# Optimization experiments

Measured on AMD Instinct MI355X. Metric: run time of the kernel, lower is better.

## Reference

```python
import jax, jax.numpy as jnp
import numpy as np

N, E, H, HEADS, L = 10000, 64000, 128, 8, 8
D = H // HEADS
CUTOFF = 5.0
EPS = 1e-5


def _xavier(key, shape):
    lim = float(np.sqrt(6.0 / (shape[0] + shape[1])))
    return jax.random.uniform(key, shape, minval=-lim, maxval=lim, dtype=jnp.float32)


def setup_inputs() -> dict:
    key = jax.random.key(0)
    ks = jax.random.split(key, 20)
    zeros = lambda *s: jnp.zeros(s, jnp.float32)
    return {
        "x": jax.random.normal(ks[0], (N, H), jnp.float32),
        "vec": 0.1 * jax.random.normal(ks[1], (N, L, H), jnp.float32),
        "f_ij": jax.random.normal(ks[2], (E, H), jnp.float32),
        "d_ij": jax.random.normal(ks[3], (E, L), jnp.float32),
        "r_ij": jax.random.uniform(ks[4], (E,), jnp.float32, 0.0, CUTOFF),
        "edge_index": jax.random.randint(ks[5], (2, E), 0, N),
        "ln_g": jnp.ones((H,), jnp.float32), "ln_b": zeros(H),
        "vln_w": jnp.ones((H,), jnp.float32),
        "W_vec": _xavier(ks[6], (H, 3 * H)),
        "W_q": _xavier(ks[7], (H, H)), "b_q": zeros(H),
        "W_k": _xavier(ks[8], (H, H)), "b_k": zeros(H),
        "W_v": _xavier(ks[9], (H, H)), "b_v": zeros(H),
        "W_dk": _xavier(ks[10], (H, H)), "b_dk": zeros(H),
        "W_dv": _xavier(ks[11], (H, H)), "b_dv": zeros(H),
        "W_s": _xavier(ks[12], (H, 2 * H)), "b_s": zeros(2 * H),
        "W_f": _xavier(ks[13], (H, H)), "b_f": zeros(H),
        "W_src": _xavier(ks[14], (H, H)),
        "W_trg": _xavier(ks[15], (H, H)),
        "W_o": _xavier(ks[16], (H, 3 * H)), "b_o": zeros(3 * H),
    }


def _layernorm(x, g, b):
    mu = jnp.mean(x, -1, keepdims=True)
    var = jnp.mean((x - mu) ** 2, -1, keepdims=True)
    return (x - mu) * jax.lax.rsqrt(var + EPS) * g + b


def _cutoff(r):
    # CosineCutoff: 0.5*(cos(pi*r/cutoff)+1) for r < cutoff
    return 0.5 * (jnp.cos(jnp.pi * r / CUTOFF) + 1.0) * (r < CUTOFF).astype(r.dtype)


def _vec_rejection(v, d):
    # v: [E, L, H], d: [E, L]; remove the component of v along d (per channel)
    proj = jnp.einsum("elh,el->eh", v, d)
    return v - proj[:, None, :] * d[:, :, None]


def reference(x, vec, f_ij, d_ij, r_ij, edge_index, ln_g, ln_b, vln_w, W_vec,
              W_q, b_q, W_k, b_k, W_v, b_v, W_dk, b_dk, W_dv, b_dv,
              W_s, b_s, W_f, b_f, W_src, W_trg, W_o, b_o):
    src, dst = edge_index[0], edge_index[1]  # j (source), i (target)
    x = _layernorm(x, ln_g, ln_b)
    vec = vec * vln_w  # VecLayerNorm with norm_type="none": identity norm * weight

    q = (x @ W_q + b_q).reshape(N, HEADS, D)
    k = (x @ W_k + b_k).reshape(N, HEADS, D)
    v = (x @ W_v + b_v).reshape(N, HEADS, D)
    dk = jax.nn.silu(f_ij @ W_dk + b_dk).reshape(E, HEADS, D)
    dv = jax.nn.silu(f_ij @ W_dv + b_dv).reshape(E, HEADS, D)

    vec1, vec2, vec3 = jnp.split(jnp.einsum("nlh,hk->nlk", vec, W_vec), 3, axis=-1)
    vec_dot = jnp.sum(vec1 * vec2, axis=1)  # [N, H]

    # ---- message (per edge) ----
    attn = jnp.sum(q[dst] * k[src] * dk, axis=-1)          # [E, HEADS]
    attn = jax.nn.silu(attn) * _cutoff(r_ij)[:, None]
    vm = (v[src] * dv * attn[:, :, None]).reshape(E, H)    # [E, H]
    s1, s2 = jnp.split(jax.nn.silu(vm @ W_s + b_s), 2, axis=-1)
    vec_m = vec[src] * s1[:, None, :] + s2[:, None, :] * d_ij[:, :, None]  # [E, L, H]

    # ---- aggregate (scatter-add to target nodes) ----
    x_agg = jax.ops.segment_sum(vm, dst, num_segments=N)       # [N, H]
    vec_agg = jax.ops.segment_sum(vec_m, dst, num_segments=N)  # [N, L, H]

    # ---- edge update ----
    w1 = _vec_rejection(jnp.einsum("elh,hk->elk", vec[dst], W_trg), d_ij)
    w2 = _vec_rejection(jnp.einsum("elh,hk->elk", vec[src], W_src), -d_ij)
    w_dot = jnp.sum(w1 * w2, axis=1)                       # [E, H]
    df_ij = jax.nn.silu(f_ij @ W_f + b_f) * w_dot

    # ---- node update ----
    o1, o2, o3 = jnp.split(x_agg @ W_o + b_o, 3, axis=-1)
    dx = vec_dot * o2 + o3
    dvec = vec3 * o1[:, None, :] + vec_agg
    return dx, dvec, df_ij
```

## Files before the change

### kernel.cpp

```cpp
#include <hip/hip_runtime.h>
#include <hip/hip_bf16.h>
#include <math.h>

#define N_NODES 10000
#define N_EDGES 64000
#define H 128
#define L 8
#define NL (N_NODES * L)

typedef __attribute__((ext_vector_type(4))) float f32x4;
typedef __attribute__((ext_vector_type(8))) __bf16 bf16x8;
typedef __attribute__((ext_vector_type(4))) __bf16 bf16x4;

__device__ __forceinline__ float silu_f(float x) { return x / (1.f + __expf(-x)); }

__global__ __launch_bounds__(256) void prep_kernel(
    const float* __restrict__ Wvec, const float* __restrict__ Wq, const float* __restrict__ Wk,
    const float* __restrict__ Wv, const float* __restrict__ Wdk, const float* __restrict__ Wdv,
    const float* __restrict__ Ws, const float* __restrict__ Wtrg, const float* __restrict__ Wsrc,
    const float* __restrict__ Wf, const float* __restrict__ Wo,
    const float* __restrict__ bq, const float* __restrict__ bk, const float* __restrict__ bv,
    const float* __restrict__ bdk, const float* __restrict__ bdv, const float* __restrict__ bf,
    __bf16* __restrict__ Wt, float* __restrict__ bqkv, float* __restrict__ bfm,
    const float* __restrict__ x, const float* __restrict__ g, const float* __restrict__ b,
    __bf16* __restrict__ xln, const float* __restrict__ vec, const float* __restrict__ w,
    __bf16* __restrict__ vecw, __bf16* __restrict__ vecwT) {
  __shared__ float tile[32][33];
  int bid = blockIdx.x;
  int t = threadIdx.x;
  if (bid < 256) {
    int ct = bid >> 2, kt = bid & 3;
    int gc0 = ct * 32;
    const float* W; int ldw, sc0;
    if      (gc0 < 384)  { W = Wvec; ldw = 384; sc0 = gc0; }
    else if (gc0 < 512)  { W = Wtrg; ldw = 128; sc0 = gc0 - 384; }
    else if (gc0 < 640)  { W = Wsrc; ldw = 128; sc0 = gc0 - 512; }
    else if (gc0 < 768)  { W = Wq;   ldw = 128; sc0 = gc0 - 640; }
    else if (gc0 < 896)  { W = Wk;   ldw = 128; sc0 = gc0 - 768; }
    else if (gc0 < 1024) { W = Wv;   ldw = 128; sc0 = gc0 - 896; }
    else if (gc0 < 1152) { W = Wdk;  ldw = 128; sc0 = gc0 - 1024; }
    else if (gc0 < 1280) { W = Wdv;  ldw = 128; sc0 = gc0 - 1152; }
    else if (gc0 < 1408) { W = Wf;   ldw = 128; sc0 = gc0 - 1280; }
    else if (gc0 < 1664) { W = Ws;   ldw = 256; sc0 = gc0 - 1408; }
    else                 { W = Wo;   ldw = 384; sc0 = gc0 - 1664; }
    int tx = t & 31, ty = t >> 5;
#pragma unroll
    for (int i = 0; i < 4; ++i)
      tile[ty + i * 8][tx] = W[(size_t)(kt * 32 + ty + i * 8) * ldw + sc0 + tx];
    __syncthreads();
#pragma unroll
    for (int i = 0; i < 4; ++i)
      Wt[(size_t)(gc0 + ty + i * 8) * 128 + kt * 32 + tx] = (__bf16)tile[tx][ty + i * 8];
  } else if (bid == 256) {
    if (t < 128) { bqkv[t] = bq[t]; bqkv[128 + t] = bk[t]; bqkv[256 + t] = bv[t]; }
  } else if (bid == 257) {
    if (t < 128) { bfm[t] = bdk[t]; bfm[128 + t] = bdv[t]; bfm[256 + t] = bf[t]; }
  } else if (bid < 258 + 5000) {
    int n = (bid - 258) * 2 + (t >> 7);
    int h = t & 127;
    float wl = w[h];
    const float* base = vec + (size_t)n * 1024 + h;
    __bf16* orow = vecw + (size_t)n * 1024 + h;
    bf16x8 pack;
#pragma unroll
    for (int l = 0; l < 8; ++l) {
      __bf16 bv = (__bf16)(base[l * 128] * wl);
      orow[l * 128] = bv;
      pack[l] = bv;
    }
    *(bf16x8*)(vecwT + (size_t)n * 1024 + h * 8) = pack;
  } else {
    int wave = t >> 6;
    int lane = t & 63;
    int n = (bid - 258 - 5000) * 4 + wave;
    if (n >= N_NODES) return;
    const float* xr = x + (size_t)n * H;
    float a0 = xr[lane], a1 = xr[lane + 64];
    float s = a0 + a1;
#pragma unroll
    for (int off = 32; off >= 1; off >>= 1) s += __shfl_xor(s, off, 64);
    float mu = s * (1.f / H);
    float d0 = a0 - mu, d1 = a1 - mu;
    float v = d0 * d0 + d1 * d1;
#pragma unroll
    for (int off = 32; off >= 1; off >>= 1) v += __shfl_xor(v, off, 64);
    float rstd = rsqrtf(v * (1.f / H) + 1e-5f);
    __bf16* orow = xln + (size_t)n * H;
    orow[lane] = (__bf16)(d0 * rstd * g[lane] + b[lane]);
    orow[lane + 64] = (__bf16)(d1 * rstd * g[lane + 64] + b[lane + 64]);
  }
}

__global__ __launch_bounds__(256) void egather_kernel(const float* __restrict__ fin,
                                                      const float* __restrict__ d_ij,
                                                      const float* __restrict__ r_ij,
                                                      const int* __restrict__ elist,
                                                      __bf16* __restrict__ fout,
                                                      float* __restrict__ d2,
                                                      float* __restrict__ r2) {
  int bid = blockIdx.x;
  if (bid < 8000) {
    int p = bid * 8 + (threadIdx.x >> 5);
    int c = (threadIdx.x & 31) * 4;
    int e = elist[p];
    f32x4 a = *(const f32x4*)(fin + (size_t)e * 128 + c);
    bf16x4 h;
    h[0] = (__bf16)a[0]; h[1] = (__bf16)a[1]; h[2] = (__bf16)a[2]; h[3] = (__bf16)a[3];
    *(bf16x4*)(fout + (size_t)p * 128 + c) = h;
  } else {
    int idx = (bid - 8000) * 256 + threadIdx.x;
    int p = idx >> 3, j = idx & 7;
    int e = elist[p];
    d2[idx] = d_ij[(size_t)e * 8 + j];
    if (j == 0) r2[p] = r_ij[e];
  }
}

__global__ __launch_bounds__(256, 2) void vdot_gemm(const __bf16* __restrict__ A,
                                                    const __bf16* __restrict__ Bt,
                                                    float* __restrict__ vdot) {
  __shared__ __bf16 As[128 * 128];
  const int tid = threadIdx.x;
  const int lane = tid & 63;
  const int wave = tid >> 6;
  const int wm = wave >> 1, wn = wave & 1;
  const int row0 = blockIdx.x * 128;

#pragma unroll
  for (int i = 0; i < 8; ++i) {
    int c = tid + i * 256;
    int row = c >> 4, k8 = c & 15;
    int k8s = k8 ^ (row & 7);
    const __bf16* src = A + (size_t)(row0 + row) * 128 + k8s * 8;
    __builtin_amdgcn_global_load_lds((const __attribute__((address_space(1))) void*)src,
                                     (__attribute__((address_space(3))) void*)(As + c * 8),
                                     16, 0, 0);
  }
  __syncthreads();

  f32x4 pacc[4][4], acc[4][4];
#pragma unroll
  for (int mi = 0; mi < 4; ++mi)
#pragma unroll
    for (int ni = 0; ni < 4; ++ni) {
      pacc[mi][ni] = f32x4{0.f, 0.f, 0.f, 0.f};
      acc[mi][ni] = f32x4{0.f, 0.f, 0.f, 0.f};
    }
#pragma unroll
  for (int ct = 0; ct < 2; ++ct) {
    const __bf16* Bbase =
        Bt + ((size_t)(ct * 128 + wn * 64 + (lane & 15)) << 7) + ((lane >> 4) << 3);
#pragma unroll
    for (int ks = 0; ks < 4; ++ks) {
      bf16x8 b[4];
#pragma unroll
      for (int ni = 0; ni < 4; ++ni) b[ni] = *(const bf16x8*)(Bbase + (ni << 11) + (ks << 5));
      bf16x8 a[4];
#pragma unroll
      for (int mi = 0; mi < 4; ++mi) {
        int row = wm * 64 + mi * 16 + (lane & 15);
        int byte = (row * 256 + ks * 64 + ((lane >> 4) << 4)) ^ ((row & 7) << 4);
        a[mi] = *(const bf16x8*)((const char*)As + byte);
      }
      if (ct == 0) {
#pragma unroll
        for (int mi = 0; mi < 4; ++mi)
#pragma unroll
          for (int ni = 0; ni < 4; ++ni)
            pacc[mi][ni] =
                __builtin_amdgcn_mfma_f32_16x16x32_bf16(a[mi], b[ni], pacc[mi][ni], 0, 0, 0);
      } else {
#pragma unroll
        for (int mi = 0; mi < 4; ++mi)
#pragma unroll
          for (int ni = 0; ni < 4; ++ni)
            acc[mi][ni] =
                __builtin_amdgcn_mfma_f32_16x16x32_bf16(a[mi], b[ni], acc[mi][ni], 0, 0, 0);
      }
    }
  }
#pragma unroll
  for (int mi = 0; mi < 4; ++mi) {
#pragma unroll
    for (int ni = 0; ni < 4; ++ni) {
      float sr = pacc[mi][ni][0] * acc[mi][ni][0] + pacc[mi][ni][1] * acc[mi][ni][1] +
                 pacc[mi][ni][2] * acc[mi][ni][2] + pacc[mi][ni][3] * acc[mi][ni][3];
      sr += __shfl_xor(sr, 16, 64);
      if ((lane & 16) == 0) {
        int node = (row0 >> 3) + wm * 8 + mi * 2 + (lane >> 5);
        int col = wn * 64 + ni * 16 + (lane & 15);
        vdot[(size_t)node * 128 + col] = sr;
      }
    }
  }
}

__global__ __launch_bounds__(256, 3) void gemm_multi(
    const __bf16* __restrict__ vecw, const __bf16* __restrict__ xln,
    const __bf16* __restrict__ fijb, const __bf16* __restrict__ Wt,
    const float* __restrict__ bqkv, const float* __restrict__ bfm,
    __bf16* __restrict__ vec3, __bf16* __restrict__ vtT, __bf16* __restrict__ vsT,
    __bf16* __restrict__ qkv, __bf16* __restrict__ fm) {
  __shared__ __bf16 As[128 * 128];
  __bf16* Cs = As;
  const int tid = threadIdx.x;
  const int lane = tid & 63;
  const int wave = tid >> 6;
  const int wm = wave >> 1, wn = wave & 1;

  int bid = blockIdx.x;
  const __bf16* A;
  const __bf16* Bt;
  const float* bias = nullptr;
  __bf16* C = nullptr;
  int nx, ny, M, ldc = 384, act = 0, big = 0;
  if (bid < 1896) {
    A = vecw; Bt = Wt + (size_t)256 * 128; nx = 625; ny = 3; M = NL; big = 1;
  } else if (bid < 2136) {
    bid -= 1896;
    A = xln; Bt = Wt + (size_t)640 * 128; bias = bqkv; C = qkv; nx = 79; ny = 3; M = N_NODES;
  } else {
    bid -= 2136;
    A = fijb; Bt = Wt + (size_t)1024 * 128; bias = bfm; C = fm; nx = 500; ny = 3; M = N_EDGES;
    act = 1;
  }

  const int xi = bid & 7;
  const int rem = bid >> 3;
  const int y = rem % ny;
  const int x = (rem / ny) * 8 + xi;
  if (x >= nx) return;
  const int row0 = x * 128;

#pragma unroll
  for (int i = 0; i < 8; ++i) {
    int c = tid + i * 256;
    int row = c >> 4, k8 = c & 15;
    int k8s = k8 ^ (row & 7);
    const __bf16* src = A + (size_t)(row0 + row) * 128 + k8s * 8;
    __builtin_amdgcn_global_load_lds((const __attribute__((address_space(1))) void*)src,
                                     (__attribute__((address_space(3))) void*)(As + c * 8),
                                     16, 0, 0);
  }
  __syncthreads();

  const __bf16* Bbase =
      Bt + ((size_t)(y * 128 + wn * 64 + (lane & 15)) << 7) + ((lane >> 4) << 3);
  bf16x8 b[4][4];
#pragma unroll
  for (int ks = 0; ks < 4; ++ks)
#pragma unroll
    for (int ni = 0; ni < 4; ++ni) b[ks][ni] = *(const bf16x8*)(Bbase + (ni << 11) + (ks << 5));

  f32x4 acc[4][4];
#pragma unroll
  for (int mi = 0; mi < 4; ++mi)
#pragma unroll
    for (int ni = 0; ni < 4; ++ni) acc[mi][ni] = f32x4{0.f, 0.f, 0.f, 0.f};

#pragma unroll
  for (int ks = 0; ks < 4; ++ks) {
    bf16x8 a[4];
#pragma unroll
    for (int mi = 0; mi < 4; ++mi) {
      int row = wm * 64 + mi * 16 + (lane & 15);
      int byte = (row * 256 + ks * 64 + ((lane >> 4) << 4)) ^ ((row & 7) << 4);
      a[mi] = *(const bf16x8*)((const char*)As + byte);
    }
#pragma unroll
    for (int mi = 0; mi < 4; ++mi)
#pragma unroll
      for (int ni = 0; ni < 4; ++ni)
        acc[mi][ni] =
            __builtin_amdgcn_mfma_f32_16x16x32_bf16(a[mi], b[ks][ni], acc[mi][ni], 0, 0, 0);
  }

  if (big) {
    __bf16* T = (y == 1) ? vtT : vsT;
#pragma unroll
    for (int p = 0; p < 2; ++p) {
      __syncthreads();
      int rl = (wm << 5) | ((lane >> 4) << 2);
#pragma unroll
      for (int q = 0; q < 2; ++q) {
        int mi = 2 * p + q;
#pragma unroll
        for (int ni = 0; ni < 4; ++ni) {
          int col = wn * 64 + ni * 16 + (lane & 15);
#pragma unroll
          for (int r = 0; r < 4; ++r)
            Cs[(rl + q * 16 + r) * 136 + col] = (__bf16)acc[mi][ni][r];
        }
      }
      __syncthreads();
      if (y == 0) {
#pragma unroll
        for (int rr = 0; rr < 4; ++rr) {
          int row = (tid >> 4) + rr * 16;
          int chunk = tid & 15;
          bf16x8 v = *(const bf16x8*)(Cs + row * 136 + chunk * 8);
          int grow = row0 + (row >> 5) * 64 + (2 * p + ((row >> 4) & 1)) * 16 + (row & 15);
          *(bf16x8*)(vec3 + (size_t)grow * 128 + chunk * 8) = v;
        }
      } else {
#pragma unroll
        for (int j = 0; j < 4; ++j) {
          int idx = tid + 256 * j;
          int node_idx = idx >> 7;
          int h = idx & 127;
          int wmm = node_idx >> 2, qq = (node_idx >> 1) & 1, w = node_idx & 1;
          int base = wmm * 32 + qq * 16 + w * 8;
          bf16x8 v;
#pragma unroll
          for (int l = 0; l < 8; ++l) v[l] = Cs[(base + l) * 136 + h];
          int g = (row0 >> 3) + wmm * 8 + (2 * p + qq) * 2 + w;
          *(bf16x8*)(T + (size_t)g * 1024 + h * 8) = v;
        }
      }
    }
  } else {
    const int cstore = y * 128;
#pragma unroll
    for (int p = 0; p < 2; ++p) {
      __syncthreads();
      int rl = (wm << 5) | ((lane >> 4) << 2);
#pragma unroll
      for (int q = 0; q < 2; ++q) {
        int mi = 2 * p + q;
#pragma unroll
        for (int ni = 0; ni < 4; ++ni) {
          int col = wn * 64 + ni * 16 + (lane & 15);
          float bv = bias[cstore + col];
#pragma unroll
          for (int r = 0; r < 4; ++r) {
            float xv = acc[mi][ni][r] + bv;
            if (act) xv = silu_f(xv);
            Cs[(rl + q * 16 + r) * 136 + col] = (__bf16)xv;
          }
        }
      }
      __syncthreads();
#pragma unroll
      for (int rr = 0; rr < 4; ++rr) {
        int row = (tid >> 4) + rr * 16;
        int chunk = tid & 15;
        bf16x8 v = *(const bf16x8*)(Cs + row * 136 + chunk * 8);
        int grow = row0 + (row >> 5) * 64 + (2 * p + ((row >> 4) & 1)) * 16 + (row & 15);
        if (grow < M)
          *(bf16x8*)(C + (size_t)grow * ldc + cstore + chunk * 8) = v;
      }
    }
  }
}

template <typename CT>
__global__ __launch_bounds__(256, 3) void gemm_v9(const __bf16* __restrict__ A,
                                                  const __bf16* __restrict__ Bt,
                                                  const float* __restrict__ bias,
                                                  CT* __restrict__ C, int M, int nx, int ny,
                                                  int ldc, int act) {
  __shared__ __bf16 As[128 * 128];
  __bf16* Cs = As;
  const int bid = blockIdx.x;
  const int xi = bid & 7;
  const int rem = bid >> 3;
  const int y = rem % ny;
  const int x = (rem / ny) * 8 + xi;
  if (x >= nx) return;
  const int tid = threadIdx.x;
  const int lane = tid & 63;
  const int wave = tid >> 6;
  const int wm = wave >> 1, wn = wave & 1;
  const int row0 = x * 128;

#pragma unroll
  for (int i = 0; i < 8; ++i) {
    int c = tid + i * 256;
    int row = c >> 4, k8 = c & 15;
    int k8s = k8 ^ (row & 7);
    const __bf16* src = A + (size_t)(row0 + row) * 128 + k8s * 8;
    __builtin_amdgcn_global_load_lds((const __attribute__((address_space(1))) void*)src,
                                     (__attribute__((address_space(3))) void*)(As + c * 8),
                                     16, 0, 0);
  }
  __syncthreads();

  const __bf16* Bbase =
      Bt + ((size_t)(y * 128 + wn * 64 + (lane & 15)) << 7) + ((lane >> 4) << 3);
  bf16x8 b[4][4];
#pragma unroll
  for (int ks = 0; ks < 4; ++ks)
#pragma unroll
    for (int ni = 0; ni < 4; ++ni) b[ks][ni] = *(const bf16x8*)(Bbase + (ni << 11) + (ks << 5));

  f32x4 acc[4][4];
#pragma unroll
  for (int mi = 0; mi < 4; ++mi)
#pragma unroll
    for (int ni = 0; ni < 4; ++ni) acc[mi][ni] = f32x4{0.f, 0.f, 0.f, 0.f};

#pragma unroll
  for (int ks = 0; ks < 4; ++ks) {
    bf16x8 a[4];
#pragma unroll
    for (int mi = 0; mi < 4; ++mi) {
      int row = wm * 64 + mi * 16 + (lane & 15);
      int byte = (row * 256 + ks * 64 + ((lane >> 4) << 4)) ^ ((row & 7) << 4);
      a[mi] = *(const bf16x8*)((const char*)As + byte);
    }
#pragma unroll
    for (int mi = 0; mi < 4; ++mi)
#pragma unroll
      for (int ni = 0; ni < 4; ++ni)
        acc[mi][ni] =
            __builtin_amdgcn_mfma_f32_16x16x32_bf16(a[mi], b[ks][ni], acc[mi][ni], 0, 0, 0);
  }

  const int cstore = y * 128;
  if constexpr (sizeof(CT) == 2) {
#pragma unroll
    for (int p = 0; p < 2; ++p) {
      __syncthreads();
      int rl = (wm << 5) | ((lane >> 4) << 2);
#pragma unroll
      for (int q = 0; q < 2; ++q) {
        int mi = 2 * p + q;
#pragma unroll
        for (int ni = 0; ni < 4; ++ni) {
          int col = wn * 64 + ni * 16 + (lane & 15);
          float bv = bias ? bias[cstore + col] : 0.f;
#pragma unroll
          for (int r = 0; r < 4; ++r) {
            float xv = acc[mi][ni][r] + bv;
            if (act) xv = silu_f(xv);
            Cs[(rl + q * 16 + r) * 136 + col] = (__bf16)xv;
          }
        }
      }
      __syncthreads();
#pragma unroll
      for (int rr = 0; rr < 4; ++rr) {
        int row = (tid >> 4) + rr * 16;
        int chunk = tid & 15;
        bf16x8 v = *(const bf16x8*)(Cs + row * 136 + chunk * 8);
        int grow = row0 + (row >> 5) * 64 + (2 * p + ((row >> 4) & 1)) * 16 + (row & 15);
        if (grow < M)
          *(bf16x8*)(C + (size_t)grow * ldc + cstore + chunk * 8) = v;
      }
    }
  } else {
#pragma unroll
    for (int mi = 0; mi < 4; ++mi) {
      int rbase = row0 + wm * 64 + mi * 16 + ((lane >> 4) << 2);
#pragma unroll
      for (int ni = 0; ni < 4; ++ni) {
        int gcol = cstore + wn * 64 + ni * 16 + (lane & 15);
        float bv = bias ? bias[cstore + wn * 64 + ni * 16 + (lane & 15)] : 0.f;
#pragma unroll
        for (int r = 0; r < 4; ++r) {
          int grow = rbase + r;
          if (grow < M) {
            float xv = acc[mi][ni][r] + bv;
            if (act) xv = silu_f(xv);
            C[(size_t)grow * ldc + gcol] = (CT)xv;
          }
        }
      }
    }
  }
}

static inline int swz_grid(int nx, int ny) { return ((nx + 7) / 8) * ny * 8; }

__global__ __launch_bounds__(256) void msg_kernel(const __bf16* __restrict__ qkv,
                                                  const __bf16* __restrict__ fm,
                                                  const float* __restrict__ r2,
                                                  const int* __restrict__ srclist,
                                                  const int* __restrict__ dstlist,
                                                  __bf16* __restrict__ vm) {
  int p = blockIdx.x * 2 + (threadIdx.x >> 7);
  int h = threadIdx.x & 127;
  int src = srclist[p], dst = dstlist[p];
  float qv = (float)qkv[(size_t)dst * 384 + h];
  float kv = (float)qkv[(size_t)src * 384 + 128 + h];
  float vv = (float)qkv[(size_t)src * 384 + 256 + h];
  float t = qv * kv * (float)fm[(size_t)p * 384 + h];
#pragma unroll
  for (int off = 8; off >= 1; off >>= 1) t += __shfl_xor(t, off, 16);
  float r = r2[p];
  float cut = 0.5f * (__cosf(0.6283185307f * r) + 1.f);
  cut = (r < 5.f) ? cut : 0.f;
  float attn = silu_f(t) * cut;
  vm[(size_t)p * H + h] = (__bf16)(vv * (float)fm[(size_t)p * 384 + 128 + h] * attn);
}

__global__ __launch_bounds__(256) void hist_kernel(const int* __restrict__ ei,
                                                   int* __restrict__ cnt) {
  int e = blockIdx.x * 256 + threadIdx.x;
  if (e < N_EDGES) atomicAdd(&cnt[ei[N_EDGES + e]], 1);
}

__global__ __launch_bounds__(1024) void scan_kernel(const int* __restrict__ cnt,
                                                    int* __restrict__ rowptr) {
  __shared__ int wsum[16];
  int t = threadIdx.x;
  int base = t * 10;
  int local[10];
  int s = 0;
#pragma unroll
  for (int i = 0; i < 10; ++i) {
    int v = (base + i < N_NODES) ? cnt[base + i] : 0;
    local[i] = s;
    s += v;
  }
  int lane = t & 63, wave = t >> 6;
  int inc = s;
#pragma unroll
  for (int off = 1; off < 64; off <<= 1) {
    int u = __shfl_up(inc, off, 64);
    if (lane >= off) inc += u;
  }
  if (lane == 63) wsum[wave] = inc;
  __syncthreads();
  if (t == 0) {
    int acc = 0;
#pragma unroll
    for (int w = 0; w < 16; ++w) { int v = wsum[w]; wsum[w] = acc; acc += v; }
  }
  __syncthreads();
  int excl = inc - s + wsum[wave];
#pragma unroll
  for (int i = 0; i < 10; ++i)
    if (base + i <= N_NODES) rowptr[base + i] = excl + local[i];
}

__global__ __launch_bounds__(256) void fill_kernel(const int* __restrict__ ei,
                                                   const int* __restrict__ rowptr,
                                                   int* __restrict__ cursor,
                                                   int* __restrict__ elist,
                                                   int* __restrict__ srclist,
                                                   int* __restrict__ dstlist) {
  int e = blockIdx.x * 256 + threadIdx.x;
  if (e < N_EDGES) {
    int s = ei[e];
    int d = ei[N_EDGES + e];
    int p = atomicAdd(&cursor[d], 1);
    int idx = rowptr[d] + p;
    elist[idx] = e;
    srclist[idx] = s;
    dstlist[idx] = d;
  }
}

__global__ __launch_bounds__(128) void node_kernel(const __bf16* __restrict__ vm,
                                                   const __bf16* __restrict__ s,
                                                   const __bf16* __restrict__ vecwT,
                                                   const __bf16* __restrict__ vtT,
                                                   const __bf16* __restrict__ vsT,
                                                   const __bf16* __restrict__ fm,
                                                   const float* __restrict__ d2,
                                                   const int* __restrict__ srclist,
                                                   const int* __restrict__ elist,
                                                   const int* __restrict__ rowptr,
                                                   __bf16* __restrict__ x_agg,
                                                   __bf16* __restrict__ avb,
                                                   float* __restrict__ df) {
  int n = blockIdx.x;
  int h = threadIdx.x;
  int beg = rowptr[n], end = rowptr[n + 1];

  bf16x8 vt8 = *(const bf16x8*)(vtT + (size_t)n * 1024 + h * 8);
  float vt[L];
#pragma unroll
  for (int l = 0; l < L; l++) vt[l] = (float)vt8[l];

  float ax = 0.f;
  float av[L] = {};
  for (int p = beg; p < end; ++p) {
    int src = srclist[p];
    const float* dd = d2 + (size_t)p * L;
    float d[L], sd2 = 0.f;
#pragma unroll
    for (int l = 0; l < L; l++) {
      d[l] = dd[l];
      sd2 += d[l] * d[l];
    }
    ax += (float)vm[(size_t)p * H + h];
    float s1 = (float)s[(size_t)p * 256 + h];
    float s2 = (float)s[(size_t)p * 256 + 128 + h];
    bf16x8 vw8 = *(const bf16x8*)(vecwT + (size_t)src * 1024 + h * 8);
    bf16x8 vs8 = *(const bf16x8*)(vsT + (size_t)src * 1024 + h * 8);
    float dot = 0.f, p1 = 0.f, p2 = 0.f;
#pragma unroll
    for (int l = 0; l < L; l++) {
      av[l] += (float)vw8[l] * s1 + s2 * d[l];
      float bb = (float)vs8[l];
      dot += vt[l] * bb;
      p1 += vt[l] * d[l];
      p2 += bb * d[l];
    }
    float wdot = dot - p1 * p2 * (2.f - sd2);
    df[(size_t)elist[p] * H + h] = (float)fm[(size_t)p * 384 + 256 + h] * wdot;
  }
  x_agg[(size_t)n * H + h] = (__bf16)ax;
  bf16x8 pack;
#pragma unroll
  for (int l = 0; l < L; l++) pack[l] = (__bf16)av[l];
  *(bf16x8*)(avb + (size_t)n * 1024 + h * 8) = pack;
}

__global__ __launch_bounds__(256) void final_kernel(const __bf16* __restrict__ o,
                                                    const float* __restrict__ vdot,
                                                    const __bf16* __restrict__ vec3,
                                                    const __bf16* __restrict__ avb,
                                                    float* __restrict__ dx,
                                                    float* __restrict__ dvec, int n_nodes) {
  int n = blockIdx.x * 2 + (threadIdx.x >> 7);
  int h = threadIdx.x & 127;
  if (n >= n_nodes) return;
  float o1 = (float)o[(size_t)n * 384 + h];
  float o2 = (float)o[(size_t)n * 384 + 128 + h];
  float o3 = (float)o[(size_t)n * 384 + 256 + h];
  dx[(size_t)n * H + h] = vdot[(size_t)n * H + h] * o2 + o3;
  bf16x8 av8 = *(const bf16x8*)(avb + (size_t)n * 1024 + h * 8);
  float* drow = dvec + (size_t)n * L * H + h;
  const __bf16* v3 = vec3 + (size_t)n * 1024 + h;
#pragma unroll
  for (int l = 0; l < L; l++) drow[l * H] = (float)av8[l] + (float)v3[l * 128] * o1;
}

extern "C" void kernel_launch(void* const* d_in, const int* in_sizes, int n_in, void* d_out,
                              int out_size, void* d_ws, size_t ws_size, hipStream_t stream) {
  const float* x = (const float*)d_in[0];
  const float* vec = (const float*)d_in[1];
  const float* f_ij = (const float*)d_in[2];
  const float* d_ij = (const float*)d_in[3];
  const float* r_ij = (const float*)d_in[4];
  const int* ei = (const int*)d_in[5];
  const float* ln_g = (const float*)d_in[6];
  const float* ln_b = (const float*)d_in[7];
  const float* vln_w = (const float*)d_in[8];
  const float* W_vec = (const float*)d_in[9];
  const float* W_q = (const float*)d_in[10];
  const float* b_q = (const float*)d_in[11];
  const float* W_k = (const float*)d_in[12];
  const float* b_k = (const float*)d_in[13];
  const float* W_v = (const float*)d_in[14];
  const float* b_v = (const float*)d_in[15];
  const float* W_dk = (const float*)d_in[16];
  const float* b_dk = (const float*)d_in[17];
  const float* W_dv = (const float*)d_in[18];
  const float* b_dv = (const float*)d_in[19];
  const float* W_s = (const float*)d_in[20];
  const float* b_s = (const float*)d_in[21];
  const float* W_f = (const float*)d_in[22];
  const float* b_f = (const float*)d_in[23];
  const float* W_src = (const float*)d_in[24];
  const float* W_trg = (const float*)d_in[25];
  const float* W_o = (const float*)d_in[26];
  const float* b_o = (const float*)d_in[27];

  float* out = (float*)d_out;
  float* dx = out;
  float* dvec = out + (size_t)N_NODES * H;
  float* df = dvec + (size_t)N_NODES * L * H;

  float* ws = (float*)d_ws;
  __bf16* vecw = (__bf16*)ws;
  __bf16* vec3 = (__bf16*)(ws + 5120000);
  __bf16* vtT = (__bf16*)(ws + 10240000);
  __bf16* vsT = (__bf16*)(ws + 15360000);
  __bf16* fm = (__bf16*)(ws + 20480000);
  __bf16* vm = (__bf16*)(ws + 32768000);
  __bf16* s_buf = (__bf16*)(ws + 36864000);
  __bf16* qkv = (__bf16*)(ws + 45056000);
  __bf16* xln = (__bf16*)(ws + 48896000);
  __bf16* xagg = (__bf16*)(ws + 49536000);
  float* vdot = ws + 50176000;
  __bf16* Wt = (__bf16*)(ws + 51456000);
  float* bqkv = ws + 51456000 + 131072;
  float* bfm = bqkv + 384;
  int* rowptr = (int*)(bfm + 384);
  int* elist = rowptr + 10001;
  int* srclist = elist + 64000;
  int* dstlist = srclist + 64000;
  int* cnt = dstlist + 64000;
  int* cursor = cnt + 10000;
  __bf16* fijb = (__bf16*)(ws + 51900000);
  __bf16* vecwT = (__bf16*)(ws + 56000000);
  float* d2 = ws + 61200000;
  float* r2 = ws + 61712000;
  __bf16* avb = (__bf16*)(ws + 61776000);

  __bf16* o_buf = qkv;

  dim3 b256(256);

  hipMemsetAsync(cnt, 0, 2 * N_NODES * sizeof(int), stream);
  hist_kernel<<<dim3((N_EDGES + 255) / 256), b256, 0, stream>>>(ei, cnt);
  scan_kernel<<<dim3(1), dim3(1024), 0, stream>>>(cnt, rowptr);
  fill_kernel<<<dim3((N_EDGES + 255) / 256), b256, 0, stream>>>(ei, rowptr, cursor, elist,
                                                                srclist, dstlist);
  egather_kernel<<<dim3(8000 + 2000), b256, 0, stream>>>(f_ij, d_ij, r_ij, elist, fijb, d2, r2);

  prep_kernel<<<dim3(258 + 5000 + 2500), b256, 0, stream>>>(
      W_vec, W_q, W_k, W_v, W_dk, W_dv, W_s, W_trg, W_src, W_f, W_o, b_q, b_k, b_v, b_dk,
      b_dv, b_f, Wt, bqkv, bfm, x, ln_g, ln_b, xln, vec, vln_w, vecw, vecwT);

  vdot_gemm<<<dim3(625), b256, 0, stream>>>(vecw, Wt, vdot);

  gemm_multi<<<dim3(1896 + 240 + 1512), b256, 0, stream>>>(vecw, xln, fijb, Wt, bqkv, bfm,
                                                           vec3, vtT, vsT, qkv, fm);

  msg_kernel<<<dim3(N_EDGES / 2), b256, 0, stream>>>(qkv, fm, r2, srclist, dstlist, vm);
  gemm_v9<__bf16><<<dim3(swz_grid(500, 2)), b256, 0, stream>>>(
      vm, Wt + (size_t)1408 * 128, b_s, s_buf, N_EDGES, 500, 2, 256, 1);
  node_kernel<<<dim3(N_NODES), dim3(128), 0, stream>>>(vm, s_buf, vecwT, vtT, vsT, fm, d2,
                                                       srclist, elist, rowptr, xagg, avb, df);
  gemm_v9<__bf16><<<dim3(swz_grid(79, 3)), b256, 0, stream>>>(
      xagg, Wt + (size_t)1664 * 128, b_o, o_buf, N_NODES, 79, 3, 384, 0);
  final_kernel<<<dim3(5000), b256, 0, stream>>>(o_buf, vdot, vec3, avb, dx, dvec, N_NODES);
}
```

Baseline: 266.4 us.

## Fuse output GEMM with final node update and merge edge gather into prep

Merges the edge-gather kernel into the prep kernel as extra block ranges, saving one launch. Replaces the output-projection GEMM and the final elementwise kernel with one kernel. Each block computes all three 128-column tiles of x_agg@W_o into shared memory and then writes dx and dvec directly, so the o buffer no longer round-trips through global memory. The tradeoff is only 79 blocks with a large LDS footprint at occupancy 1, which lowers parallelism for the bandwidth-heavy dvec write. The gemm_v9 float-output epilogue branch is also removed.

```diff
diff --git a/kernel.cpp b/kernel.cpp
--- a/kernel.cpp
+++ b/kernel.cpp
@@ -14,7 +14,7 @@
 
 __device__ __forceinline__ float silu_f(float x) { return x / (1.f + __expf(-x)); }
 
-__global__ __launch_bounds__(256) void prep_kernel(
+__global__ __launch_bounds__(256) void prep2_kernel(
     const float* __restrict__ Wvec, const float* __restrict__ Wq, const float* __restrict__ Wk,
     const float* __restrict__ Wv, const float* __restrict__ Wdk, const float* __restrict__ Wdv,
     const float* __restrict__ Ws, const float* __restrict__ Wtrg, const float* __restrict__ Wsrc,
@@ -24,7 +24,10 @@
     __bf16* __restrict__ Wt, float* __restrict__ bqkv, float* __restrict__ bfm,
     const float* __restrict__ x, const float* __restrict__ g, const float* __restrict__ b,
     __bf16* __restrict__ xln, const float* __restrict__ vec, const float* __restrict__ w,
-    __bf16* __restrict__ vecw, __bf16* __restrict__ vecwT) {
+    __bf16* __restrict__ vecw, __bf16* __restrict__ vecwT,
+    const float* __restrict__ fin, const float* __restrict__ d_ij,
+    const float* __restrict__ r_ij, const int* __restrict__ elist,
+    __bf16* __restrict__ fout, float* __restrict__ d2, float* __restrict__ r2) {
   __shared__ float tile[32][33];
   int bid = blockIdx.x;
   int t = threadIdx.x;
@@ -69,7 +72,7 @@
       pack[l] = bv;
     }
     *(bf16x8*)(vecwT + (size_t)n * 1024 + h * 8) = pack;
-  } else {
+  } else if (bid < 258 + 5000 + 2500) {
     int wave = t >> 6;
     int lane = t & 63;
     int n = (bid - 258 - 5000) * 4 + wave;
@@ -88,27 +91,16 @@
     __bf16* orow = xln + (size_t)n * H;
     orow[lane] = (__bf16)(d0 * rstd * g[lane] + b[lane]);
     orow[lane + 64] = (__bf16)(d1 * rstd * g[lane + 64] + b[lane + 64]);
-  }
-}
-
-__global__ __launch_bounds__(256) void egather_kernel(const float* __restrict__ fin,
-                                                      const float* __restrict__ d_ij,
-                                                      const float* __restrict__ r_ij,
-                                                      const int* __restrict__ elist,
-                                                      __bf16* __restrict__ fout,
-                                                      float* __restrict__ d2,
-                                                      float* __restrict__ r2) {
-  int bid = blockIdx.x;
-  if (bid < 8000) {
-    int p = bid * 8 + (threadIdx.x >> 5);
-    int c = (threadIdx.x & 31) * 4;
+  } else if (bid < 258 + 5000 + 2500 + 8000) {
+    int p = (bid - 7758) * 8 + (t >> 5);
+    int c = (t & 31) * 4;
     int e = elist[p];
     f32x4 a = *(const f32x4*)(fin + (size_t)e * 128 + c);
     bf16x4 h;
     h[0] = (__bf16)a[0]; h[1] = (__bf16)a[1]; h[2] = (__bf16)a[2]; h[3] = (__bf16)a[3];
     *(bf16x4*)(fout + (size_t)p * 128 + c) = h;
   } else {
-    int idx = (bid - 8000) * 256 + threadIdx.x;
+    int idx = (bid - 15758) * 256 + t;
     int p = idx >> 3, j = idx & 7;
     int e = elist[p];
     d2[idx] = d_ij[(size_t)e * 8 + j];
@@ -417,55 +409,130 @@
   }
 
   const int cstore = y * 128;
-  if constexpr (sizeof(CT) == 2) {
-#pragma unroll
-    for (int p = 0; p < 2; ++p) {
-      __syncthreads();
-      int rl = (wm << 5) | ((lane >> 4) << 2);
-#pragma unroll
-      for (int q = 0; q < 2; ++q) {
-        int mi = 2 * p + q;
-#pragma unroll
-        for (int ni = 0; ni < 4; ++ni) {
-          int col = wn * 64 + ni * 16 + (lane & 15);
-          float bv = bias ? bias[cstore + col] : 0.f;
-#pragma unroll
-          for (int r = 0; r < 4; ++r) {
-            float xv = acc[mi][ni][r] + bv;
-            if (act) xv = silu_f(xv);
-            Cs[(rl + q * 16 + r) * 136 + col] = (__bf16)xv;
-          }
+#pragma unroll
+  for (int p = 0; p < 2; ++p) {
+    __syncthreads();
+    int rl = (wm << 5) | ((lane >> 4) << 2);
+#pragma unroll
+    for (int q = 0; q < 2; ++q) {
+      int mi = 2 * p + q;
+#pragma unroll
+      for (int ni = 0; ni < 4; ++ni) {
+        int col = wn * 64 + ni * 16 + (lane & 15);
+        float bv = bias ? bias[cstore + col] : 0.f;
+#pragma unroll
+        for (int r = 0; r < 4; ++r) {
+          float xv = acc[mi][ni][r] + bv;
+          if (act) xv = silu_f(xv);
+          Cs[(rl + q * 16 + r) * 136 + col] = (__bf16)xv;
         }
       }
-      __syncthreads();
-#pragma unroll
-      for (int rr = 0; rr < 4; ++rr) {
-        int row = (tid >> 4) + rr * 16;
-        int chunk = tid & 15;
-        bf16x8 v = *(const bf16x8*)(Cs + row * 136 + chunk * 8);
-        int grow = row0 + (row >> 5) * 64 + (2 * p + ((row >> 4) & 1)) * 16 + (row & 15);
-        if (grow < M)
-          *(bf16x8*)(C + (size_t)grow * ldc + cstore + chunk * 8) = v;
-      }
-    }
-  } else {
+    }
+    __syncthreads();
+#pragma unroll
+    for (int rr = 0; rr < 4; ++rr) {
+      int row = (tid >> 4) + rr * 16;
+      int chunk = tid & 15;
+      bf16x8 v = *(const bf16x8*)(Cs + row * 136 + chunk * 8);
+      int grow = row0 + (row >> 5) * 64 + (2 * p + ((row >> 4) & 1)) * 16 + (row & 15);
+      if (grow < M)
+        *(bf16x8*)(C + (size_t)grow * ldc + cstore + chunk * 8) = v;
+    }
+  }
+}
+
+__global__ __launch_bounds__(256, 1) void gemm_ofinal(
+    const __bf16* __restrict__ A,
+    const __bf16* __restrict__ Bt,
+    const float* __restrict__ bias,
+    const float* __restrict__ vdot,
+    const __bf16* __restrict__ vec3,
+    const __bf16* __restrict__ avb,
+    float* __restrict__ dx, float* __restrict__ dvec) {
+  __shared__ __bf16 As[128 * 128];
+  __shared__ __bf16 Os[128 * 392];
+  const int tid = threadIdx.x;
+  const int lane = tid & 63;
+  const int wave = tid >> 6;
+  const int wm = wave >> 1, wn = wave & 1;
+  const int row0 = blockIdx.x * 128;
+
+#pragma unroll
+  for (int i = 0; i < 8; ++i) {
+    int c = tid + i * 256;
+    int row = c >> 4, k8 = c & 15;
+    int k8s = k8 ^ (row & 7);
+    const __bf16* src = A + (size_t)(row0 + row) * 128 + k8s * 8;
+    __builtin_amdgcn_global_load_lds((const __attribute__((address_space(1))) void*)src,
+                                     (__attribute__((address_space(3))) void*)(As + c * 8),
+                                     16, 0, 0);
+  }
+  __syncthreads();
+
+#pragma unroll
+  for (int ct = 0; ct < 3; ++ct) {
+    const __bf16* Bbase =
+        Bt + ((size_t)(ct * 128 + wn * 64 + (lane & 15)) << 7) + ((lane >> 4) << 3);
+    bf16x8 b[4][4];
+#pragma unroll
+    for (int ks = 0; ks < 4; ++ks)
+#pragma unroll
+      for (int ni = 0; ni < 4; ++ni) b[ks][ni] = *(const bf16x8*)(Bbase + (ni << 11) + (ks << 5));
+
+    f32x4 acc[4][4];
+#pragma unroll
+    for (int mi = 0; mi < 4; ++mi)
+#pragma unroll
+      for (int ni = 0; ni < 4; ++ni) acc[mi][ni] = f32x4{0.f, 0.f, 0.f, 0.f};
+
+#pragma unroll
+    for (int ks = 0; ks < 4; ++ks) {
+      bf16x8 a[4];
+#pragma unroll
+      for (int mi = 0; mi < 4; ++mi) {
+        int row = wm * 64 + mi * 16 + (lane & 15);
+        int byte = (row * 256 + ks * 64 + ((lane >> 4) << 4)) ^ ((row & 7) << 4);
+        a[mi] = *(const bf16x8*)((const char*)As + byte);
+      }
+#pragma unroll
+      for (int mi = 0; mi < 4; ++mi)
+#pragma unroll
+        for (int ni = 0; ni < 4; ++ni)
+          acc[mi][ni] =
+              __builtin_amdgcn_mfma_f32_16x16x32_bf16(a[mi], b[ks][ni], acc[mi][ni], 0, 0, 0);
+    }
+
 #pragma unroll
     for (int mi = 0; mi < 4; ++mi) {
-      int rbase = row0 + wm * 64 + mi * 16 + ((lane >> 4) << 2);
+      int rbase = wm * 64 + mi * 16 + ((lane >> 4) << 2);
 #pragma unroll
       for (int ni = 0; ni < 4; ++ni) {
-        int gcol = cstore + wn * 64 + ni * 16 + (lane & 15);
-        float bv = bias ? bias[cstore + wn * 64 + ni * 16 + (lane & 15)] : 0.f;
-#pragma unroll
-        for (int r = 0; r < 4; ++r) {
-          int grow = rbase + r;
-          if (grow < M) {
-            float xv = acc[mi][ni][r] + bv;
-            if (act) xv = silu_f(xv);
-            C[(size_t)grow * ldc + gcol] = (CT)xv;
-          }
-        }
-      }
+        int col = ct * 128 + wn * 64 + ni * 16 + (lane & 15);
+        float bv = bias[col];
+#pragma unroll
+        for (int r = 0; r < 4; ++r)
+          Os[(rbase + r) * 392 + col] = (__bf16)(acc[mi][ni][r] + bv);
+      }
+    }
+  }
+  __syncthreads();
+
+#pragma unroll
+  for (int i = 0; i < 64; ++i) {
+    int idx = tid + i * 256;
+    int rloc = idx >> 7;
+    int h = idx & 127;
+    int n = row0 + rloc;
+    if (n < N_NODES) {
+      float o1 = (float)Os[rloc * 392 + h];
+      float o2 = (float)Os[rloc * 392 + 128 + h];
+      float o3 = (float)Os[rloc * 392 + 256 + h];
+      dx[(size_t)n * H + h] = vdot[(size_t)n * 128 + h] * o2 + o3;
+      bf16x8 av8 = *(const bf16x8*)(avb + (size_t)n * 1024 + h * 8);
+      const __bf16* v3 = vec3 + (size_t)n * 1024 + h;
+      float* drow = dvec + (size_t)n * 1024 + h;
+#pragma unroll
+      for (int l = 0; l < L; l++) drow[l * 128] = (float)av8[l] + (float)v3[l * 128] * o1;
     }
   }
 }
@@ -607,26 +674,6 @@
 #pragma unroll
   for (int l = 0; l < L; l++) pack[l] = (__bf16)av[l];
   *(bf16x8*)(avb + (size_t)n * 1024 + h * 8) = pack;
-}
-
-__global__ __launch_bounds__(256) void final_kernel(const __bf16* __restrict__ o,
-                                                    const float* __restrict__ vdot,
-                                                    const __bf16* __restrict__ vec3,
-                                                    const __bf16* __restrict__ avb,
-                                                    float* __restrict__ dx,
-                                                    float* __restrict__ dvec, int n_nodes) {
-  int n = blockIdx.x * 2 + (threadIdx.x >> 7);
-  int h = threadIdx.x & 127;
-  if (n >= n_nodes) return;
-  float o1 = (float)o[(size_t)n * 384 + h];
-  float o2 = (float)o[(size_t)n * 384 + 128 + h];
-  float o3 = (float)o[(size_t)n * 384 + 256 + h];
-  dx[(size_t)n * H + h] = vdot[(size_t)n * H + h] * o2 + o3;
-  bf16x8 av8 = *(const bf16x8*)(avb + (size_t)n * 1024 + h * 8);
-  float* drow = dvec + (size_t)n * L * H + h;
-  const __bf16* v3 = vec3 + (size_t)n * 1024 + h;
-#pragma unroll
-  for (int l = 0; l < L; l++) drow[l * H] = (float)av8[l] + (float)v3[l * 128] * o1;
 }
 
 extern "C" void kernel_launch(void* const* d_in, const int* in_sizes, int n_in, void* d_out,
@@ -692,8 +739,6 @@
   float* r2 = ws + 61712000;
   __bf16* avb = (__bf16*)(ws + 61776000);
 
-  __bf16* o_buf = qkv;
-
   dim3 b256(256);
 
   hipMemsetAsync(cnt, 0, 2 * N_NODES * sizeof(int), stream);
@@ -701,11 +746,10 @@
   scan_kernel<<<dim3(1), dim3(1024), 0, stream>>>(cnt, rowptr);
   fill_kernel<<<dim3((N_EDGES + 255) / 256), b256, 0, stream>>>(ei, rowptr, cursor, elist,
                                                                 srclist, dstlist);
-  egather_kernel<<<dim3(8000 + 2000), b256, 0, stream>>>(f_ij, d_ij, r_ij, elist, fijb, d2, r2);
-
-  prep_kernel<<<dim3(258 + 5000 + 2500), b256, 0, stream>>>(
+  prep2_kernel<<<dim3(17758), b256, 0, stream>>>(
       W_vec, W_q, W_k, W_v, W_dk, W_dv, W_s, W_trg, W_src, W_f, W_o, b_q, b_k, b_v, b_dk,
-      b_dv, b_f, Wt, bqkv, bfm, x, ln_g, ln_b, xln, vec, vln_w, vecw, vecwT);
+      b_dv, b_f, Wt, bqkv, bfm, x, ln_g, ln_b, xln, vec, vln_w, vecw, vecwT, f_ij, d_ij,
+      r_ij, elist, fijb, d2, r2);
 
   vdot_gemm<<<dim3(625), b256, 0, stream>>>(vecw, Wt, vdot);
 
@@ -717,7 +761,6 @@
       vm, Wt + (size_t)1408 * 128, b_s, s_buf, N_EDGES, 500, 2, 256, 1);
   node_kernel<<<dim3(N_NODES), dim3(128), 0, stream>>>(vm, s_buf, vecwT, vtT, vsT, fm, d2,
                                                        srclist, elist, rowptr, xagg, avb, df);
-  gemm_v9<__bf16><<<dim3(swz_grid(79, 3)), b256, 0, stream>>>(
-      xagg, Wt + (size_t)1664 * 128, b_o, o_buf, N_NODES, 79, 3, 384, 0);
-  final_kernel<<<dim3(5000), b256, 0, stream>>>(o_buf, vdot, vec3, avb, dx, dvec, N_NODES);
-}
+  gemm_ofinal<<<dim3(79), b256, 0, stream>>>(xagg, Wt + (size_t)1664 * 128, b_o, vdot, vec3,
+                                             avb, dx, dvec);
+}
```

Result: slower. 298.9 us (+12.2%).
